# Performance work log

Hardware: AMD Instinct MI355X
Metric: run time of the kernel (lower is better)

## Reference

```python
import jax, jax.numpy as jnp
import numpy as np

B, T, D = 2, 2048, 1024
H, RANK = 16, 16
HD = D // H  # 64


def setup_inputs() -> dict:
    key = jax.random.key(0)
    ks = jax.random.split(key, 10)
    x = jax.random.normal(ks[0], (B, T, D), dtype=jnp.float32)
    def lin(k):
        kw, kb = jax.random.split(k)
        W = jax.random.normal(kw, (D, D), dtype=jnp.float32) * (1.0 / np.sqrt(D))
        b = jax.random.normal(kb, (D,), dtype=jnp.float32) * 0.01
        return W, b
    Wq, bq = lin(ks[1])
    Wk, bk = lin(ks[2])
    Wv, bv = lin(ks[3])
    Wo, bo = lin(ks[4])
    # per-head low-rank metric factors A_h: (min(rank, head_dim), head_dim)
    A = jax.random.normal(ks[5], (H, min(RANK, HD), HD), dtype=jnp.float32) * 0.02
    log_lambda = jnp.full((H,), jnp.log(jnp.float32(0.1)), dtype=jnp.float32)
    return {"x": x, "Wq": Wq, "bq": bq, "Wk": Wk, "bk": bk,
            "Wv": Wv, "bv": bv, "Wo": Wo, "bo": bo,
            "A": A, "log_lambda": log_lambda}


def reference(x, Wq, bq, Wk, bk, Wv, bv, Wo, bo, A, log_lambda):
    b, t, d = x.shape
    h = A.shape[0]
    hd = d // h

    def split_heads(y):
        return y.reshape(b, t, h, hd).transpose(0, 2, 1, 3)  # (b,h,t,hd)

    q = split_heads(x @ Wq.T + bq)
    k = split_heads(x @ Wk.T + bk)
    v = split_heads(x @ Wv.T + bv)

    # Metric g_h = A_h^T A_h + lam_h * I. torch.einsum('btid,dd,btjd->btj')
    # uses only diag(g) and sums over i: dist[b,t,j] = sum_d S[b,t,d]*gdiag[d]*diff[b,t,j,d]
    # where S[b,t,d] = sum_i (q[b,t,d] - k[b,i,d]) = t*q - sum_i k.
    gdiag = jnp.sum(A * A, axis=1) + jnp.exp(log_lambda)[:, None]  # (h,hd)

    ksum = jnp.sum(k, axis=2)                      # (b,h,hd)
    S = jnp.float32(t) * q - ksum[:, :, None, :]   # (b,h,t,hd)
    Sg = S * gdiag[None, :, None, :]               # (b,h,t,hd)
    c = jnp.sum(Sg * q, axis=-1)                   # (b,h,t)
    # dist_sq[b,h,t,j] = c[b,h,t] - sum_d Sg[b,h,t,d] * k[b,h,j,d]
    dist_sq = c[..., None] - jnp.einsum('bhtd,bhjd->bhtj', Sg, k)
    attn = jax.nn.softmax(-dist_sq, axis=-1)       # (b,h,t,t)
    o = jnp.einsum('bhtj,bhjd->bhtd', attn, v)     # (b,h,t,hd)
    out = o.transpose(0, 2, 1, 3).reshape(b, t, d)
    return out @ Wo.T + bo
```

## Files before the change

kernel.cpp:

```cpp
#include <hip/hip_runtime.h>
#include <math.h>

#define D_MODEL 1024
#define NHEAD   16
#define HDIM    64
#define SEQ     2048
#define BATCH   2
#define NROWS   (BATCH*SEQ)

typedef unsigned short u16;
typedef __attribute__((ext_vector_type(4))) unsigned short u16x4;
typedef __attribute__((ext_vector_type(8))) short short8;
typedef __attribute__((ext_vector_type(4))) float f32x4;
typedef __attribute__((ext_vector_type(2))) unsigned int u32x2;

#define SWZ(row, c) (((c) ^ ((row) & 7)) * 8)
#define GF(row) ((((row) + ((row) >> 2))) & 3)

__device__ __forceinline__ u16 f2bf(float x) {
    unsigned int u = __float_as_uint(x);
    u += 0x7fffu + ((u >> 16) & 1u);
    return (u16)(u >> 16);
}
__device__ __forceinline__ float bf2f(u16 h) {
    return __uint_as_float(((unsigned int)h) << 16);
}
__device__ __forceinline__ unsigned int cvt_pk_bf16(float a, float b) {
    unsigned int r;
    asm("v_cvt_pk_bf16_f32 %0, %1, %2" : "=v"(r) : "v"(a), "v"(b));
    return r;
}
__device__ __forceinline__ void st8(u16* p, short8 v) {
    u16x4 a, b;
    a[0]=(u16)v[0]; a[1]=(u16)v[1]; a[2]=(u16)v[2]; a[3]=(u16)v[3];
    b[0]=(u16)v[4]; b[1]=(u16)v[5]; b[2]=(u16)v[6]; b[3]=(u16)v[7];
    *(u16x4*)p = a; *(u16x4*)(p + 4) = b;
}
__device__ __forceinline__ void gld16(const u16* g, u16* l) {
    __builtin_amdgcn_global_load_lds(
        (const __attribute__((address_space(1))) void*)g,
        (__attribute__((address_space(3))) void*)l, 16, 0, 0);
}

__global__ void gdiag_kernel(const float* __restrict__ A,
                             const float* __restrict__ log_lambda,
                             float* __restrict__ gdiag) {
    int id = blockIdx.x * 256 + threadIdx.x;
    if (id >= NHEAD * HDIM) return;
    int h = id >> 6, d = id & 63;
    float s = 0.f;
#pragma unroll
    for (int i = 0; i < 16; ++i) {
        float a = A[(h * 16 + i) * HDIM + d];
        s += a * a;
    }
    gdiag[id] = (s + __expf(log_lambda[h])) * 1.4426950408889634f;
}

__global__ void prep_split(const float* __restrict__ x,
                           const float* __restrict__ Wq, const float* __restrict__ Wk,
                           const float* __restrict__ Wv, const float* __restrict__ Wo,
                           u16* __restrict__ xh, u16* __restrict__ xl,
                           u16* __restrict__ wqh, u16* __restrict__ wql,
                           u16* __restrict__ wkh, u16* __restrict__ wkl,
                           u16* __restrict__ wvh, u16* __restrict__ woh) {
    int seg = blockIdx.y;
    int i = blockIdx.x * 256 + threadIdx.x;
    const float* src; u16* dh; u16* dl; int n4;
    if      (seg == 0) { src = x;  dh = xh;  dl = xl;      n4 = NROWS * D_MODEL / 4; }
    else if (seg == 1) { src = Wq; dh = wqh; dl = wql;     n4 = D_MODEL * D_MODEL / 4; }
    else if (seg == 2) { src = Wk; dh = wkh; dl = wkl;     n4 = D_MODEL * D_MODEL / 4; }
    else if (seg == 3) { src = Wv; dh = wvh; dl = nullptr; n4 = D_MODEL * D_MODEL / 4; }
    else               { src = Wo; dh = woh; dl = nullptr; n4 = D_MODEL * D_MODEL / 4; }
    if (i >= n4) return;
    float4 v = *(const float4*)&src[(size_t)i * 4];
    float vv[4] = {v.x, v.y, v.z, v.w};
    u16x4 hv, lv;
#pragma unroll
    for (int j = 0; j < 4; ++j) {
        u16 hb = f2bf(vv[j]);
        hv[j] = hb;
        lv[j] = f2bf(vv[j] - bf2f(hb));
    }
    *(u16x4*)&dh[(size_t)i * 4] = hv;
    if (dl) *(u16x4*)&dl[(size_t)i * 4] = lv;
}

template<int NP3>
__global__ __launch_bounds__(256)
void gemm_mfma(const u16* __restrict__ Ah, const u16* __restrict__ Al,
               const u16* __restrict__ BhA, const u16* __restrict__ BlA, const float* __restrict__ biasA,
               float* outfA, u16* auxhA, u16* auxlA, float* ksumA,
               const u16* __restrict__ BhB, const u16* __restrict__ BlB, const float* __restrict__ biasB,
               float* outfB, u16* auxhB, u16* auxlB, float* ksumB,
               int out_layout) {
    const int z = blockIdx.z;
    const u16* Bh = (z == 0) ? BhA : BhB;
    const u16* Bl = (z == 0) ? BlA : BlB;
    const float* bias = (z == 0) ? biasA : biasB;
    float* outf = (z == 0) ? outfA : outfB;
    u16* auxh   = (z == 0) ? auxhA : auxhB;
    u16* auxl   = (z == 0) ? auxlA : auxlB;
    float* ksump= (z == 0) ? ksumA : ksumB;

    __shared__ __align__(16) u16 As_h[128][32], Bs_h[128][32];
    __shared__ __align__(16) u16 As_l[NP3 ? 128 : 1][32], Bs_l[NP3 ? 128 : 1][32];

    const int tid = threadIdx.x;
    const int w = tid >> 6, lane = tid & 63, quad = lane >> 4, n16 = lane & 15;
    const int rBase = blockIdx.y * 128;
    const int cBase = blockIdx.x * 128;

    const int srow0 = w * 32 + (lane >> 2);
    const int srow1 = srow0 + 16;
    const int sc0 = ((lane & 3) ^ GF(srow0)) * 8;
    const int sc1 = ((lane & 3) ^ GF(srow1)) * 8;

    f32x4 acc[2][8] = {};

    for (int kt = 0; kt < D_MODEL; kt += 32) {
        gld16(&Ah[(size_t)(rBase + srow0) * D_MODEL + kt + sc0], &As_h[w * 32][0]);
        gld16(&Ah[(size_t)(rBase + srow1) * D_MODEL + kt + sc1], &As_h[w * 32 + 16][0]);
        gld16(&Bh[(size_t)(cBase + srow0) * D_MODEL + kt + sc0], &Bs_h[w * 32][0]);
        gld16(&Bh[(size_t)(cBase + srow1) * D_MODEL + kt + sc1], &Bs_h[w * 32 + 16][0]);
        if (NP3) {
            gld16(&Al[(size_t)(rBase + srow0) * D_MODEL + kt + sc0], &As_l[w * 32][0]);
            gld16(&Al[(size_t)(rBase + srow1) * D_MODEL + kt + sc1], &As_l[w * 32 + 16][0]);
            gld16(&Bl[(size_t)(cBase + srow0) * D_MODEL + kt + sc0], &Bs_l[w * 32][0]);
            gld16(&Bl[(size_t)(cBase + srow1) * D_MODEL + kt + sc1], &Bs_l[w * 32 + 16][0]);
        }
        __syncthreads();

        short8 a_h[2], a_l[2];
#pragma unroll
        for (int mt = 0; mt < 2; ++mt) {
            const int row = w * 32 + mt * 16 + n16;
            const int cc = (quad ^ GF(row)) * 8;
            a_h[mt] = *(const short8*)&As_h[row][cc];
            if (NP3) a_l[mt] = *(const short8*)&As_l[NP3 ? row : 0][cc];
        }
#pragma unroll
        for (int nt = 0; nt < 8; ++nt) {
            const int row = nt * 16 + n16;
            const int cc = (quad ^ GF(row)) * 8;
            short8 b_h = *(const short8*)&Bs_h[row][cc];
            short8 b_l;
            if (NP3) b_l = *(const short8*)&Bs_l[NP3 ? row : 0][cc];
#pragma unroll
            for (int mt = 0; mt < 2; ++mt) {
                acc[mt][nt] = __builtin_amdgcn_mfma_f32_16x16x32_bf16(a_h[mt], b_h, acc[mt][nt], 0, 0, 0);
                if (NP3) {
                    acc[mt][nt] = __builtin_amdgcn_mfma_f32_16x16x32_bf16(a_h[mt], b_l, acc[mt][nt], 0, 0, 0);
                    acc[mt][nt] = __builtin_amdgcn_mfma_f32_16x16x32_bf16(a_l[mt], b_h, acc[mt][nt], 0, 0, 0);
                }
            }
        }
        __syncthreads();
    }

    float csum[8];
#pragma unroll
    for (int nt = 0; nt < 8; ++nt) csum[nt] = 0.f;
#pragma unroll
    for (int mt = 0; mt < 2; ++mt) {
#pragma unroll
        for (int nt = 0; nt < 8; ++nt) {
            int c = cBase + nt * 16 + n16;
            float bc = bias[c];
            int rb = rBase + w * 32 + mt * 16 + quad * 4;
#pragma unroll
            for (int reg = 0; reg < 4; ++reg) {
                float val = acc[mt][nt][reg] + bc;
                int rr = rb + reg;
                size_t idx = out_layout
                    ? ((size_t)(((rr >> 11) * NHEAD + (c >> 6)) * SEQ + (rr & (SEQ - 1)))) * HDIM + (c & 63)
                    : (size_t)rr * D_MODEL + c;
                if (outf) outf[idx] = val;
                if (auxh) {
                    u16 hb = f2bf(val);
                    auxh[idx] = hb;
                    if (auxl) auxl[idx] = f2bf(val - bf2f(hb));
                }
                csum[nt] += val;
            }
        }
    }
    if (ksump) {
#pragma unroll
        for (int nt = 0; nt < 8; ++nt) {
            float cs = csum[nt];
            cs += __shfl_xor(cs, 16);
            cs += __shfl_xor(cs, 32);
            if (quad == 0) {
                int c = cBase + nt * 16 + n16;
                int bb = rBase >> 11;
                atomicAdd(&ksump[(bb * NHEAD + (c >> 6)) * HDIM + (c & 63)], cs);
            }
        }
    }
}

__global__ __launch_bounds__(256)
void vtrans_kernel(const u16* __restrict__ vh, u16* __restrict__ vT) {
    __shared__ u16 tile[64][72];
    const int tid = threadIdx.x;
    const int t0 = blockIdx.x * 64;
    const int bh = blockIdx.y;
    const u16* vp = vh + (size_t)bh * SEQ * HDIM;
#pragma unroll
    for (int s = 0; s < 2; ++s) {
        int id = s * 256 + tid;
        int row = id >> 3, c8 = (id & 7) * 8;
        st8(&tile[row][c8], *(const short8*)&vp[(size_t)(t0 + row) * HDIM + c8]);
    }
    __syncthreads();
#pragma unroll
    for (int s = 0; s < 2; ++s) {
        int id = s * 256 + tid;
        int d = id >> 3, t8 = (id & 7) * 8;
        short8 r;
#pragma unroll
        for (int i = 0; i < 8; ++i) r[i] = (short)tile[t8 + i][d];
        *(short8*)&vT[((size_t)bh * HDIM + d) * SEQ + t0 + t8] = r;
    }
}

__global__ __launch_bounds__(256, 2)
void flash_mfma(const float* __restrict__ q, const u16* __restrict__ kh,
                const u16* __restrict__ kl, const u16* __restrict__ vT,
                const float* __restrict__ ksum, const float* __restrict__ gdiag,
                u16* __restrict__ o) {
    __shared__ __align__(16) u16 khs[2][64][64], kls[2][64][64], vTs[2][64][64];
    __shared__ __align__(16) u16 ps[4][32][64];

    const int tid = threadIdx.x;
    const int w = tid >> 6, lane = tid & 63, quad = lane >> 4, n16 = lane & 15;
    const int t0 = blockIdx.x * 128;
    const int h = blockIdx.y, b = blockIdx.z;
    const size_t bh = (size_t)b * NHEAD + h;
    const float* qp = q + bh * SEQ * HDIM;
    const u16* khp = kh + bh * SEQ * HDIM;
    const u16* klp = kl + bh * SEQ * HDIM;
    const u16* vtp = vT + bh * HDIM * SEQ;

    short8 sgh[2][2], sgl[2][2];
#pragma unroll
    for (int mt = 0; mt < 2; ++mt) {
        int qrow = t0 + w * 32 + mt * 16 + n16;
#pragma unroll
        for (int kc = 0; kc < 2; ++kc) {
            int d0 = kc * 32 + quad * 8;
            float4 q0 = *(const float4*)&qp[(size_t)qrow * HDIM + d0];
            float4 q1 = *(const float4*)&qp[(size_t)qrow * HDIM + d0 + 4];
            float4 k0 = *(const float4*)&ksum[bh * HDIM + d0];
            float4 k1 = *(const float4*)&ksum[bh * HDIM + d0 + 4];
            float4 g0 = *(const float4*)&gdiag[(size_t)h * HDIM + d0];
            float4 g1 = *(const float4*)&gdiag[(size_t)h * HDIM + d0 + 4];
            float sg[8];
            sg[0] = (2048.f * q0.x - k0.x) * g0.x; sg[1] = (2048.f * q0.y - k0.y) * g0.y;
            sg[2] = (2048.f * q0.z - k0.z) * g0.z; sg[3] = (2048.f * q0.w - k0.w) * g0.w;
            sg[4] = (2048.f * q1.x - k1.x) * g1.x; sg[5] = (2048.f * q1.y - k1.y) * g1.y;
            sg[6] = (2048.f * q1.z - k1.z) * g1.z; sg[7] = (2048.f * q1.w - k1.w) * g1.w;
#pragma unroll
            for (int j = 0; j < 8; ++j) {
                u16 hb = f2bf(sg[j]);
                sgh[mt][kc][j] = (short)hb;
                sgl[mt][kc][j] = (short)f2bf(sg[j] - bf2f(hb));
            }
        }
    }

    f32x4 oaccv[2][4] = {};
    float m_n[2] = {-INFINITY, -INFINITY};
    float l_n[2] = {0.f, 0.f};

    const int srow = tid >> 3;
    const int sc   = tid & 7;
    const int scg  = sc * 8;
    const int scl  = SWZ(srow, sc);

    short8 rk0h = *(const short8*)&khp[(size_t)srow * HDIM + scg];
    short8 rk1h = *(const short8*)&khp[(size_t)(srow + 32) * HDIM + scg];
    short8 rk0l = *(const short8*)&klp[(size_t)srow * HDIM + scg];
    short8 rk1l = *(const short8*)&klp[(size_t)(srow + 32) * HDIM + scg];
    short8 rv0  = *(const short8*)&vtp[(size_t)srow * SEQ + scg];
    short8 rv1  = *(const short8*)&vtp[(size_t)(srow + 32) * SEQ + scg];
    *(short8*)&khs[0][srow][scl] = rk0h;  *(short8*)&khs[0][srow + 32][scl] = rk1h;
    *(short8*)&kls[0][srow][scl] = rk0l;  *(short8*)&kls[0][srow + 32][scl] = rk1l;
    *(short8*)&vTs[0][srow][scl] = rv0;   *(short8*)&vTs[0][srow + 32][scl] = rv1;

    int cur = 0;
    for (int j0 = 0; j0 < SEQ; j0 += 64, cur ^= 1) {
        __syncthreads();
        const int jn = j0 + 64;
        const bool pf = (jn < SEQ);
        if (pf) {
            rk0h = *(const short8*)&khp[(size_t)(jn + srow) * HDIM + scg];
            rk1h = *(const short8*)&khp[(size_t)(jn + srow + 32) * HDIM + scg];
            rk0l = *(const short8*)&klp[(size_t)(jn + srow) * HDIM + scg];
            rk1l = *(const short8*)&klp[(size_t)(jn + srow + 32) * HDIM + scg];
            rv0  = *(const short8*)&vtp[(size_t)srow * SEQ + jn + scg];
            rv1  = *(const short8*)&vtp[(size_t)(srow + 32) * SEQ + jn + scg];
        }

        f32x4 lgT[2][4] = {};
#pragma unroll
        for (int kc = 0; kc < 2; ++kc) {
#pragma unroll
            for (int nt = 0; nt < 4; ++nt) {
                const int row = nt * 16 + n16;
                const int cc = SWZ(row, kc * 4 + quad);
                short8 b_h = *(const short8*)&khs[cur][row][cc];
                short8 b_l = *(const short8*)&kls[cur][row][cc];
#pragma unroll
                for (int mt = 0; mt < 2; ++mt) {
                    lgT[mt][nt] = __builtin_amdgcn_mfma_f32_16x16x32_bf16(b_h, sgh[mt][kc], lgT[mt][nt], 0, 0, 0);
                    lgT[mt][nt] = __builtin_amdgcn_mfma_f32_16x16x32_bf16(b_l, sgh[mt][kc], lgT[mt][nt], 0, 0, 0);
                    lgT[mt][nt] = __builtin_amdgcn_mfma_f32_16x16x32_bf16(b_h, sgl[mt][kc], lgT[mt][nt], 0, 0, 0);
                }
            }
        }

        float mx[2];
#pragma unroll
        for (int mt = 0; mt < 2; ++mt) {
            float m0 = fmaxf(fmaxf(lgT[mt][0][0], lgT[mt][0][1]), lgT[mt][0][2]);
            m0 = fmaxf(fmaxf(m0, lgT[mt][0][3]), lgT[mt][1][0]);
            m0 = fmaxf(fmaxf(m0, lgT[mt][1][1]), lgT[mt][1][2]);
            m0 = fmaxf(fmaxf(m0, lgT[mt][1][3]), lgT[mt][2][0]);
            m0 = fmaxf(fmaxf(m0, lgT[mt][2][1]), lgT[mt][2][2]);
            m0 = fmaxf(fmaxf(m0, lgT[mt][2][3]), lgT[mt][3][0]);
            m0 = fmaxf(fmaxf(m0, lgT[mt][3][1]), lgT[mt][3][2]);
            m0 = fmaxf(m0, lgT[mt][3][3]);
            m0 = fmaxf(m0, __shfl_xor(m0, 16));
            mx[mt] = fmaxf(m0, __shfl_xor(m0, 32));
        }

        const float need = fmaxf(mx[0] - m_n[0], mx[1] - m_n[1]);
        if (!__all(need <= 8.f)) {
#pragma unroll
            for (int mt = 0; mt < 2; ++mt) {
                const float mn = fmaxf(m_n[mt], mx[mt]);
                const float alpha = exp2f(m_n[mt] - mn);
                m_n[mt] = mn;
                l_n[mt] *= alpha;
                const float a0 = __shfl(alpha, quad * 4 + 0);
                const float a1 = __shfl(alpha, quad * 4 + 1);
                const float a2 = __shfl(alpha, quad * 4 + 2);
                const float a3 = __shfl(alpha, quad * 4 + 3);
#pragma unroll
                for (int nt = 0; nt < 4; ++nt) {
                    oaccv[mt][nt][0] *= a0; oaccv[mt][nt][1] *= a1;
                    oaccv[mt][nt][2] *= a2; oaccv[mt][nt][3] *= a3;
                }
            }
        }

#pragma unroll
        for (int mt = 0; mt < 2; ++mt) {
            const int prow = mt * 16 + n16;
            const float mn = m_n[mt];
            float psum = 0.f;
#pragma unroll
            for (int nt = 0; nt < 4; ++nt) {
#pragma unroll
                for (int r = 0; r < 4; ++r) lgT[mt][nt][r] = exp2f(lgT[mt][nt][r] - mn);
                u32x2 pk;
                pk[0] = cvt_pk_bf16(lgT[mt][nt][0], lgT[mt][nt][1]);
                pk[1] = cvt_pk_bf16(lgT[mt][nt][2], lgT[mt][nt][3]);
                *(u32x2*)&ps[w][prow][SWZ(prow, nt * 2 + (quad >> 1)) + (quad & 1) * 4] = pk;
                psum += (lgT[mt][nt][0] + lgT[mt][nt][1]) + (lgT[mt][nt][2] + lgT[mt][nt][3]);
            }
            l_n[mt] += psum;
        }

        short8 pa[2][2];
#pragma unroll
        for (int mt = 0; mt < 2; ++mt) {
            const int prow = mt * 16 + n16;
            pa[mt][0] = *(const short8*)&ps[w][prow][SWZ(prow, quad)];
            pa[mt][1] = *(const short8*)&ps[w][prow][SWZ(prow, quad + 4)];
        }
#pragma unroll
        for (int nt = 0; nt < 4; ++nt) {
            const int row = nt * 16 + n16;
            short8 v0 = *(const short8*)&vTs[cur][row][SWZ(row, quad)];
            short8 v1 = *(const short8*)&vTs[cur][row][SWZ(row, quad + 4)];
#pragma unroll
            for (int mt = 0; mt < 2; ++mt) {
                oaccv[mt][nt] = __builtin_amdgcn_mfma_f32_16x16x32_bf16(pa[mt][0], v0, oaccv[mt][nt], 0, 0, 0);
                oaccv[mt][nt] = __builtin_amdgcn_mfma_f32_16x16x32_bf16(pa[mt][1], v1, oaccv[mt][nt], 0, 0, 0);
            }
        }

        if (pf) {
            const int nx = cur ^ 1;
            *(short8*)&khs[nx][srow][scl] = rk0h;  *(short8*)&khs[nx][srow + 32][scl] = rk1h;
            *(short8*)&kls[nx][srow][scl] = rk0l;  *(short8*)&kls[nx][srow + 32][scl] = rk1l;
            *(short8*)&vTs[nx][srow][scl] = rv0;   *(short8*)&vTs[nx][srow + 32][scl] = rv1;
        }
    }

#pragma unroll
    for (int mt = 0; mt < 2; ++mt) {
        float l = l_n[mt];
        l += __shfl_xor(l, 16);
        l += __shfl_xor(l, 32);
        l_n[mt] = l;
    }
#pragma unroll
    for (int mt = 0; mt < 2; ++mt) {
#pragma unroll
        for (int r = 0; r < 4; ++r) {
            float lr = __shfl(l_n[mt], quad * 4 + r);
            float inv = 1.f / lr;
            int t = t0 + w * 32 + mt * 16 + quad * 4 + r;
#pragma unroll
            for (int nt = 0; nt < 4; ++nt) {
                int d = nt * 16 + n16;
                o[((size_t)(b * SEQ + t)) * D_MODEL + h * HDIM + d] = f2bf(oaccv[mt][nt][r] * inv);
            }
        }
    }
}

extern "C" void kernel_launch(void* const* d_in, const int* in_sizes, int n_in,
                              void* d_out, int out_size, void* d_ws, size_t ws_size,
                              hipStream_t stream) {
    const float* x  = (const float*)d_in[0];
    const float* Wq = (const float*)d_in[1];
    const float* bq = (const float*)d_in[2];
    const float* Wk = (const float*)d_in[3];
    const float* bk = (const float*)d_in[4];
    const float* Wv = (const float*)d_in[5];
    const float* bv = (const float*)d_in[6];
    const float* Wo = (const float*)d_in[7];
    const float* bo = (const float*)d_in[8];
    const float* A  = (const float*)d_in[9];
    const float* ll = (const float*)d_in[10];
    float* out = (float*)d_out;

    const size_t NQKV = (size_t)NROWS * D_MODEL;
    const size_t NW = (size_t)D_MODEL * D_MODEL;
    char* base = (char*)d_ws;
    float* q_ws = (float*)base;            base += NQKV * 4;
    u16* xh  = (u16*)base;                 base += NQKV * 2;
    u16* xl  = (u16*)base;                 base += NQKV * 2;
    u16* khw = (u16*)base;                 base += NQKV * 2;
    u16* klw = (u16*)base;                 base += NQKV * 2;
    u16* vhw = (u16*)base;                 base += NQKV * 2;
    u16* wqh = (u16*)base;                 base += NW * 2;
    u16* wql = (u16*)base;                 base += NW * 2;
    u16* wkh = (u16*)base;                 base += NW * 2;
    u16* wkl = (u16*)base;                 base += NW * 2;
    u16* wvh = (u16*)base;                 base += NW * 2;
    u16* woh = (u16*)base;                 base += NW * 2;
    float* gd_ws   = (float*)base;         base += NHEAD * HDIM * 4;
    float* ksum_ws = (float*)base;         base += BATCH * NHEAD * HDIM * 4;

    hipMemsetAsync(ksum_ws, 0, BATCH * NHEAD * HDIM * sizeof(float), stream);

    prep_split<<<dim3(4096, 5), 256, 0, stream>>>(x, Wq, Wk, Wv, Wo,
                                                  xh, xl, wqh, wql, wkh, wkl, wvh, woh);
    gdiag_kernel<<<4, 256, 0, stream>>>(A, ll, gd_ws);

    gemm_mfma<1><<<dim3(8, 32, 2), 256, 0, stream>>>(
        xh, xl,
        wqh, wql, bq, q_ws, nullptr, nullptr, nullptr,
        wkh, wkl, bk, nullptr, khw, klw, ksum_ws,
        1);
    gemm_mfma<0><<<dim3(8, 32, 1), 256, 0, stream>>>(
        xh, nullptr,
        wvh, nullptr, bv, nullptr, vhw, nullptr, nullptr,
        wvh, nullptr, bv, nullptr, vhw, nullptr, nullptr,
        1);

    u16* vTw = xl;
    u16* ohw = xh;
    vtrans_kernel<<<dim3(SEQ / 64, BATCH * NHEAD), 256, 0, stream>>>(vhw, vTw);

    flash_mfma<<<dim3(SEQ / 128, NHEAD, BATCH), 256, 0, stream>>>(
        q_ws, khw, klw, vTw, ksum_ws, gd_ws, ohw);

    gemm_mfma<0><<<dim3(8, 32, 1), 256, 0, stream>>>(
        ohw, nullptr,
        woh, nullptr, bo, out, nullptr, nullptr, nullptr,
        woh, nullptr, bo, out, nullptr, nullptr, nullptr,
        0);
}
```

Baseline: 307.5 us.

## Shrink GEMM tile to 128x64 with 8 waves each owning 16 rows

```diff
diff --git a/kernel.cpp b/kernel.cpp
--- a/kernel.cpp
+++ b/kernel.cpp
@@ -87,7 +87,7 @@
 }
 
 template<int NP3>
-__global__ __launch_bounds__(256)
+__global__ __launch_bounds__(512, 4)
 void gemm_mfma(const u16* __restrict__ Ah, const u16* __restrict__ Al,
                const u16* __restrict__ BhA, const u16* __restrict__ BlA, const float* __restrict__ biasA,
                float* outfA, u16* auxhA, u16* auxlA, float* ksumA,
@@ -103,91 +103,83 @@
     u16* auxl   = (z == 0) ? auxlA : auxlB;
     float* ksump= (z == 0) ? ksumA : ksumB;
 
-    __shared__ __align__(16) u16 As_h[128][32], Bs_h[128][32];
-    __shared__ __align__(16) u16 As_l[NP3 ? 128 : 1][32], Bs_l[NP3 ? 128 : 1][32];
+    __shared__ __align__(16) u16 As_h[128][32], Bs_h[64][32];
+    __shared__ __align__(16) u16 As_l[NP3 ? 128 : 1][32], Bs_l[NP3 ? 64 : 1][32];
 
     const int tid = threadIdx.x;
     const int w = tid >> 6, lane = tid & 63, quad = lane >> 4, n16 = lane & 15;
     const int rBase = blockIdx.y * 128;
-    const int cBase = blockIdx.x * 128;
-
-    const int srow0 = w * 32 + (lane >> 2);
-    const int srow1 = srow0 + 16;
-    const int sc0 = ((lane & 3) ^ GF(srow0)) * 8;
-    const int sc1 = ((lane & 3) ^ GF(srow1)) * 8;
-
-    f32x4 acc[2][8] = {};
+    const int cBase = blockIdx.x * 64;
+
+    const int lrow = lane >> 2;
+    const int lch  = lane & 3;
+    const int arow = w * 16 + lrow;
+    const int asc  = ((lch ^ GF(arow)) * 8);
+    const int brow = (w & 3) * 16 + lrow;
+    const int bsc  = ((lch ^ GF(brow)) * 8);
+
+    f32x4 acc[4] = {};
 
     for (int kt = 0; kt < D_MODEL; kt += 32) {
-        gld16(&Ah[(size_t)(rBase + srow0) * D_MODEL + kt + sc0], &As_h[w * 32][0]);
-        gld16(&Ah[(size_t)(rBase + srow1) * D_MODEL + kt + sc1], &As_h[w * 32 + 16][0]);
-        gld16(&Bh[(size_t)(cBase + srow0) * D_MODEL + kt + sc0], &Bs_h[w * 32][0]);
-        gld16(&Bh[(size_t)(cBase + srow1) * D_MODEL + kt + sc1], &Bs_h[w * 32 + 16][0]);
-        if (NP3) {
-            gld16(&Al[(size_t)(rBase + srow0) * D_MODEL + kt + sc0], &As_l[w * 32][0]);
-            gld16(&Al[(size_t)(rBase + srow1) * D_MODEL + kt + sc1], &As_l[w * 32 + 16][0]);
-            gld16(&Bl[(size_t)(cBase + srow0) * D_MODEL + kt + sc0], &Bs_l[w * 32][0]);
-            gld16(&Bl[(size_t)(cBase + srow1) * D_MODEL + kt + sc1], &Bs_l[w * 32 + 16][0]);
+        gld16(&Ah[(size_t)(rBase + arow) * D_MODEL + kt + asc], &As_h[w * 16][0]);
+        if (NP3) gld16(&Al[(size_t)(rBase + arow) * D_MODEL + kt + asc], &As_l[w * 16][0]);
+        if (w < 4) {
+            gld16(&Bh[(size_t)(cBase + brow) * D_MODEL + kt + bsc], &Bs_h[(w & 3) * 16][0]);
+        } else if (NP3) {
+            gld16(&Bl[(size_t)(cBase + brow) * D_MODEL + kt + bsc], &Bs_l[NP3 ? (w & 3) * 16 : 0][0]);
         }
         __syncthreads();
 
-        short8 a_h[2], a_l[2];
-#pragma unroll
-        for (int mt = 0; mt < 2; ++mt) {
-            const int row = w * 32 + mt * 16 + n16;
+        short8 a_h, a_l;
+        {
+            const int row = w * 16 + n16;
             const int cc = (quad ^ GF(row)) * 8;
-            a_h[mt] = *(const short8*)&As_h[row][cc];
-            if (NP3) a_l[mt] = *(const short8*)&As_l[NP3 ? row : 0][cc];
-        }
-#pragma unroll
-        for (int nt = 0; nt < 8; ++nt) {
+            a_h = *(const short8*)&As_h[row][cc];
+            if (NP3) a_l = *(const short8*)&As_l[NP3 ? row : 0][cc];
+        }
+#pragma unroll
+        for (int nt = 0; nt < 4; ++nt) {
             const int row = nt * 16 + n16;
             const int cc = (quad ^ GF(row)) * 8;
             short8 b_h = *(const short8*)&Bs_h[row][cc];
             short8 b_l;
             if (NP3) b_l = *(const short8*)&Bs_l[NP3 ? row : 0][cc];
-#pragma unroll
-            for (int mt = 0; mt < 2; ++mt) {
-                acc[mt][nt] = __builtin_amdgcn_mfma_f32_16x16x32_bf16(a_h[mt], b_h, acc[mt][nt], 0, 0, 0);
-                if (NP3) {
-                    acc[mt][nt] = __builtin_amdgcn_mfma_f32_16x16x32_bf16(a_h[mt], b_l, acc[mt][nt], 0, 0, 0);
-                    acc[mt][nt] = __builtin_amdgcn_mfma_f32_16x16x32_bf16(a_l[mt], b_h, acc[mt][nt], 0, 0, 0);
-                }
+            acc[nt] = __builtin_amdgcn_mfma_f32_16x16x32_bf16(a_h, b_h, acc[nt], 0, 0, 0);
+            if (NP3) {
+                acc[nt] = __builtin_amdgcn_mfma_f32_16x16x32_bf16(a_h, b_l, acc[nt], 0, 0, 0);
+                acc[nt] = __builtin_amdgcn_mfma_f32_16x16x32_bf16(a_l, b_h, acc[nt], 0, 0, 0);
             }
         }
         __syncthreads();
     }
 
-    float csum[8];
-#pragma unroll
-    for (int nt = 0; nt < 8; ++nt) csum[nt] = 0.f;
-#pragma unroll
-    for (int mt = 0; mt < 2; ++mt) {
-#pragma unroll
-        for (int nt = 0; nt < 8; ++nt) {
-            int c = cBase + nt * 16 + n16;
-            float bc = bias[c];
-            int rb = rBase + w * 32 + mt * 16 + quad * 4;
-#pragma unroll
-            for (int reg = 0; reg < 4; ++reg) {
-                float val = acc[mt][nt][reg] + bc;
-                int rr = rb + reg;
-                size_t idx = out_layout
-                    ? ((size_t)(((rr >> 11) * NHEAD + (c >> 6)) * SEQ + (rr & (SEQ - 1)))) * HDIM + (c & 63)
-                    : (size_t)rr * D_MODEL + c;
-                if (outf) outf[idx] = val;
-                if (auxh) {
-                    u16 hb = f2bf(val);
-                    auxh[idx] = hb;
-                    if (auxl) auxl[idx] = f2bf(val - bf2f(hb));
-                }
-                csum[nt] += val;
-            }
+    float csum[4];
+#pragma unroll
+    for (int nt = 0; nt < 4; ++nt) csum[nt] = 0.f;
+#pragma unroll
+    for (int nt = 0; nt < 4; ++nt) {
+        int c = cBase + nt * 16 + n16;
+        float bc = bias[c];
+        int rb = rBase + w * 16 + quad * 4;
+#pragma unroll
+        for (int reg = 0; reg < 4; ++reg) {
+            float val = acc[nt][reg] + bc;
+            int rr = rb + reg;
+            size_t idx = out_layout
+                ? ((size_t)(((rr >> 11) * NHEAD + (c >> 6)) * SEQ + (rr & (SEQ - 1)))) * HDIM + (c & 63)
+                : (size_t)rr * D_MODEL + c;
+            if (outf) outf[idx] = val;
+            if (auxh) {
+                u16 hb = f2bf(val);
+                auxh[idx] = hb;
+                if (auxl) auxl[idx] = f2bf(val - bf2f(hb));
+            }
+            csum[nt] += val;
         }
     }
     if (ksump) {
 #pragma unroll
-        for (int nt = 0; nt < 8; ++nt) {
+        for (int nt = 0; nt < 4; ++nt) {
             float cs = csum[nt];
             cs += __shfl_xor(cs, 16);
             cs += __shfl_xor(cs, 32);
@@ -464,12 +456,12 @@
                                                   xh, xl, wqh, wql, wkh, wkl, wvh, woh);
     gdiag_kernel<<<4, 256, 0, stream>>>(A, ll, gd_ws);
 
-    gemm_mfma<1><<<dim3(8, 32, 2), 256, 0, stream>>>(
+    gemm_mfma<1><<<dim3(16, 32, 2), 512, 0, stream>>>(
         xh, xl,
         wqh, wql, bq, q_ws, nullptr, nullptr, nullptr,
         wkh, wkl, bk, nullptr, khw, klw, ksum_ws,
         1);
-    gemm_mfma<0><<<dim3(8, 32, 1), 256, 0, stream>>>(
+    gemm_mfma<0><<<dim3(16, 32, 1), 512, 0, stream>>>(
         xh, nullptr,
         wvh, nullptr, bv, nullptr, vhw, nullptr, nullptr,
         wvh, nullptr, bv, nullptr, vhw, nullptr, nullptr,
@@ -482,7 +474,7 @@
     flash_mfma<<<dim3(SEQ / 128, NHEAD, BATCH), 256, 0, stream>>>(
         q_ws, khw, klw, vTw, ksum_ws, gd_ws, ohw);
 
-    gemm_mfma<0><<<dim3(8, 32, 1), 256, 0, stream>>>(
+    gemm_mfma<0><<<dim3(16, 32, 1), 512, 0, stream>>>(
         ohw, nullptr,
         woh, nullptr, bo, out, nullptr, nullptr, nullptr,
         woh, nullptr, bo, out, nullptr, nullptr, nullptr,
```

New measurement: 303.1 us. Within noise of the previous version (-1.4%).
